# Optimization experiments

Hardware: AMD Instinct MI355X
Metric: run time of the kernel (lower is better)

Reference implementation:

```python
import jax, jax.numpy as jnp
import numpy as np

N_NODES = 100000
N_EDGES = 1600000
HIDDEN = 128
NUM_RBF = 50
NTYPES = 95
CUTOFF = 5.0


def setup_inputs() -> dict:
    key = jax.random.key(0)
    ks = jax.random.split(key, 10)
    z = jax.random.randint(ks[0], (N_NODES,), 0, NTYPES)
    node_feat = jax.random.normal(ks[1], (N_NODES, HIDDEN), dtype=jnp.float32)
    edge_index = jax.random.randint(ks[2], (2, N_EDGES), 0, N_NODES)
    # distances uniform in [0, 6) so some edges fall beyond the 5.0 cutoff
    edge_weight = jax.random.uniform(ks[3], (N_EDGES,), dtype=jnp.float32) * 6.0
    edge_attr = jax.random.normal(ks[4], (N_EDGES, NUM_RBF), dtype=jnp.float32)
    # learned parameters
    emb = jax.random.normal(ks[5], (NTYPES, HIDDEN), dtype=jnp.float32)
    dp_w = jax.random.normal(ks[6], (HIDDEN, NUM_RBF), dtype=jnp.float32) * (1.0 / np.sqrt(NUM_RBF))
    dp_b = jnp.zeros((HIDDEN,), dtype=jnp.float32)
    comb_w = jax.random.normal(ks[7], (HIDDEN, 2 * HIDDEN), dtype=jnp.float32) * (1.0 / np.sqrt(2 * HIDDEN))
    comb_b = jnp.zeros((HIDDEN,), dtype=jnp.float32)
    return {"z": z, "node_feat": node_feat, "edge_index": edge_index,
            "edge_weight": edge_weight, "edge_attr": edge_attr,
            "emb": emb, "dp_w": dp_w, "dp_b": dp_b,
            "comb_w": comb_w, "comb_b": comb_b}


def cosine_cutoff(r, cutoff):
    c = 0.5 * (jnp.cos(r * (jnp.pi / cutoff)) + 1.0)
    return jnp.where(r < cutoff, c, 0.0)


def reference(z, node_feat, edge_index, edge_weight, edge_attr,
              emb, dp_w, dp_b, comb_w, comb_b):
    # distance filter: [E, H]
    C = cosine_cutoff(edge_weight, CUTOFF)
    W = (edge_attr @ dp_w.T + dp_b) * C[:, None]
    # neighbor-type embedding gathered per edge destination
    x_nb = emb[z]                      # [N, H]
    msg = W * x_nb[edge_index[1]]      # [E, H]
    # scatter-add messages to source nodes
    agg = jnp.zeros_like(node_feat).at[edge_index[0]].add(msg)  # [N, H]
    # combine node features with aggregated neighborhood embedding
    out = jnp.concatenate([node_feat, agg], axis=1) @ comb_w.T + comb_b
    return out
```

## Files before the change

### kernel.cpp

```cpp
#include <hip/hip_runtime.h>

#define HIDDEN 128
#define NRBF 50
#define CUTOFF_F 5.0f
#define PI_OVER_CUTOFF 0.6283185307179586f
#define EPB 512
#define B_PITCH 35
#define W_PITCH 66
#define A_PITCH 68

typedef _Float16 half8_t __attribute__((ext_vector_type(8)));
using f32x4_t  = __attribute__((ext_vector_type(4))) float;
using short8_t = __attribute__((ext_vector_type(8))) short;
typedef __attribute__((ext_vector_type(2))) _Float16 hf2;

static __device__ __forceinline__ unsigned int pkh(float a, float b) {
    return __builtin_bit_cast(unsigned int, __builtin_amdgcn_cvt_pkrtz(a, b));
}
static __device__ __forceinline__ float cvlo(unsigned int u) {
    return (float)__builtin_bit_cast(hf2, u)[0];
}
static __device__ __forceinline__ float cvhi(unsigned int u) {
    return (float)__builtin_bit_cast(hf2, u)[1];
}
static __device__ __forceinline__ unsigned int pk_bf16(float a, float b) {
    unsigned int ua = __float_as_uint(a), ub = __float_as_uint(b);
    ua = (ua + 0x7FFFu + ((ua >> 16) & 1u)) >> 16;
    ub = (ub + 0x7FFFu + ((ub >> 16) & 1u)) >> 16;
    return ua | (ub << 16);
}
static __device__ __forceinline__ void loadd16(const int4* p, int t, int* s) {
    int4 q0 = p[t * 4], q1 = p[t * 4 + 1], q2 = p[t * 4 + 2], q3 = p[t * 4 + 3];
    s[0]  = __builtin_amdgcn_readfirstlane(q0.x);
    s[1]  = __builtin_amdgcn_readfirstlane(q0.y);
    s[2]  = __builtin_amdgcn_readfirstlane(q0.z);
    s[3]  = __builtin_amdgcn_readfirstlane(q0.w);
    s[4]  = __builtin_amdgcn_readfirstlane(q1.x);
    s[5]  = __builtin_amdgcn_readfirstlane(q1.y);
    s[6]  = __builtin_amdgcn_readfirstlane(q1.z);
    s[7]  = __builtin_amdgcn_readfirstlane(q1.w);
    s[8]  = __builtin_amdgcn_readfirstlane(q2.x);
    s[9]  = __builtin_amdgcn_readfirstlane(q2.y);
    s[10] = __builtin_amdgcn_readfirstlane(q2.z);
    s[11] = __builtin_amdgcn_readfirstlane(q2.w);
    s[12] = __builtin_amdgcn_readfirstlane(q3.x);
    s[13] = __builtin_amdgcn_readfirstlane(q3.y);
    s[14] = __builtin_amdgcn_readfirstlane(q3.z);
    s[15] = __builtin_amdgcn_readfirstlane(q3.w);
}


__global__ __launch_bounds__(256) void hist_kernel(
    const int* __restrict__ ei, const float* __restrict__ ew,
    int* __restrict__ cnt, int E)
{
    int e = blockIdx.x * 256 + threadIdx.x;
    if (e >= E) return;
    float r = ew[e];
    if (r < CUTOFF_F) atomicAdd(&cnt[ei[e]], 1);
}

__global__ __launch_bounds__(256) void scan1_kernel(
    const int* __restrict__ cnt, int* __restrict__ rowptr,
    int* __restrict__ bsum, int N)
{
    __shared__ int sh[256];
    int t = threadIdx.x, b = blockIdx.x;
    int base = b * 1024 + t * 4;
    int v[4];
#pragma unroll
    for (int j = 0; j < 4; ++j) v[j] = (base + j < N) ? cnt[base + j] : 0;
    int s = v[0] + v[1] + v[2] + v[3];
    sh[t] = s;
    __syncthreads();
    for (int off = 1; off < 256; off <<= 1) {
        int x = (t >= off) ? sh[t - off] : 0;
        __syncthreads();
        sh[t] += x;
        __syncthreads();
    }
    int run = sh[t] - s;
#pragma unroll
    for (int j = 0; j < 4; ++j) {
        if (base + j < N) rowptr[base + j] = run;
        run += v[j];
    }
    if (t == 255) bsum[b] = sh[255];
}

__global__ __launch_bounds__(256) void scan2_kernel(
    int* __restrict__ bsum, int* __restrict__ rowptr, int nb, int N)
{
    __shared__ int sh[256];
    int t = threadIdx.x;
    int v = (t < nb) ? bsum[t] : 0;
    sh[t] = v;
    __syncthreads();
    for (int off = 1; off < 256; off <<= 1) {
        int x = (t >= off) ? sh[t - off] : 0;
        __syncthreads();
        sh[t] += x;
        __syncthreads();
    }
    if (t < nb) bsum[t] = sh[t] - v;
    if (t == 255) rowptr[N] = sh[255];
}

__global__ __launch_bounds__(256) void scan3_kernel(
    int* __restrict__ rowptr, int* __restrict__ woff,
    const int* __restrict__ bsum, int N)
{
    int t = threadIdx.x, b = blockIdx.x;
    int base = b * 1024 + t * 4;
    int off = bsum[b];
#pragma unroll
    for (int j = 0; j < 4; ++j) {
        int i = base + j;
        if (i < N) {
            int r = rowptr[i] + off;
            rowptr[i] = r;
            woff[i] = r;
        }
    }
}

__global__ __launch_bounds__(256) void pad_kernel(
    const int* __restrict__ rowptr, int N,
    int* __restrict__ desc, int* __restrict__ eidA, float* __restrict__ CA)
{
    int M = rowptr[N];
    int t = blockIdx.x * 256 + threadIdx.x;
    if (t < 512) { desc[M + t] = 0; eidA[M + t] = 0; CA[M + t] = 0.f; }
}

__global__ __launch_bounds__(256) void pack_emb(
    const float* __restrict__ emb, unsigned int* __restrict__ embp, int NT)
{
    int i = blockIdx.x * 256 + threadIdx.x;
    if (i >= NT * 64) return;
    int t = i >> 6, j = i & 63;
    embp[i] = pkh(emb[t * HIDDEN + j], emb[t * HIDDEN + j + 64]);
}

__global__ __launch_bounds__(256) void scatter_slim(
    const int* __restrict__ z, const int* __restrict__ ei,
    const float* __restrict__ ew, int* __restrict__ woff,
    int* __restrict__ desc, int* __restrict__ eidA, float* __restrict__ CA,
    int E)
{
    int e = blockIdx.x * 256 + threadIdx.x;
    if (e >= E) return;
    float r = ew[e];
    if (!(r < CUTOFF_F)) return;
    float C = 0.5f * (cosf(r * PI_OVER_CUTOFF) + 1.0f);
    int src = ei[e];
    int dst = ei[E + e];
    int zt  = z[dst];
    int p = atomicAdd(&woff[src], 1);
    desc[p] = src | (zt << 20);
    eidA[p] = e;
    CA[p]   = C;
}

__global__ __launch_bounds__(256) void gather_mfma(
    const int* __restrict__ rowptr, const int* __restrict__ desc,
    const int* __restrict__ eidA, const float* __restrict__ CA,
    const float* __restrict__ ea, const unsigned int* __restrict__ embp,
    const float* __restrict__ dpw, const float* __restrict__ dpb,
    float* __restrict__ agg, int N)
{
    __shared__ unsigned int Blds[128 * B_PITCH];
    __shared__ float        Ast[4][16 * A_PITCH];
    __shared__ unsigned int Wlds[4][16 * W_PITCH];
    int M = rowptr[N];

    int nwg = gridDim.x, orig = blockIdx.x;
    int q = nwg >> 3, r8 = nwg & 7, xcd = orig & 7, sub = orig >> 3;
    int lb = (xcd < r8) ? xcd * (q + 1) + sub
                        : r8 * (q + 1) + (xcd - r8) * q + sub;
    int gbase = lb * EPB;
    if (gbase >= M) return;

    int tid  = threadIdx.x;
    int w    = tid >> 6;
    int lane = tid & 63;
    int c    = lane & 15;
    int g    = lane >> 4;
    int lidx = min(lane, 49);

    for (int idx = tid; idx < 128 * 32; idx += 256) {
        int h = idx >> 5, p = idx & 31;
        unsigned int u = 0u;
        if (p < 25) {
            float2 v = *(const float2*)(dpw + h * NRBF + 2 * p);
            u = pkh(v.x, v.y);
        } else if (p == 25) {
            u = pkh(dpb[h], 0.f);
        }
        Blds[h * B_PITCH + p] = u;
    }
    __syncthreads();

    float*        AstW = Ast[w];
    unsigned int* Ww   = Wlds[w];
    int wbeg = gbase + w * 128;
    if (wbeg >= M) return;

    bool runc;
    if (wbeg == 0) runc = true;
    else runc = ((desc[wbeg - 1] & 0xFFFFF) != (desc[wbeg] & 0xFFFFF));

    const int4* dp = (const int4*)(desc + wbeg);
    const int4* ep = (const int4*)(eidA + wbeg);

    int sd[16], se[16], sdN[16], seN[16];
    float vr[16], vrN[16];

    loadd16(dp, 0, sd);
    loadd16(ep, 0, se);
    float vC = CA[wbeg + c];
#pragma unroll
    for (int j = 0; j < 16; ++j)
        vr[j] = ea[(size_t)(unsigned int)se[j] * NRBF + lidx];
    loadd16(dp, 1, sdN);
    loadd16(ep, 1, seN);
    float vCN = CA[wbeg + 16 + c];

    int   cur = -1;
    float r0 = 0.f, r1 = 0.f;

    for (int t = 0; t < 8; ++t) {
        if (t < 7) {
#pragma unroll
            for (int j = 0; j < 16; ++j)
                vrN[j] = ea[(size_t)(unsigned int)seN[j] * NRBF + lidx];
        }
        unsigned int evp[16];
#pragma unroll
        for (int j = 0; j < 16; ++j)
            evp[j] = embp[(((unsigned int)sd[j]) >> 20) * 64 + lane];

#pragma unroll
        for (int j = 0; j < 16; ++j)
            AstW[j * A_PITCH + lane] = vr[j];

        const float* ab = &AstW[c * A_PITCH];
        float4 f0 = *(const float4*)&ab[g * 8];
        float4 f1 = *(const float4*)&ab[g * 8 + 4];
        uint4 A0u = make_uint4(pkh(vC * f0.x, vC * f0.y), pkh(vC * f0.z, vC * f0.w),
                               pkh(vC * f1.x, vC * f1.y), pkh(vC * f1.z, vC * f1.w));
        uint4 A1u;
        if (g < 2) {
            float4 h0 = *(const float4*)&ab[32 + g * 8];
            float4 h1 = *(const float4*)&ab[36 + g * 8];
            A1u = make_uint4(pkh(vC * h0.x, vC * h0.y), pkh(vC * h0.z, vC * h0.w),
                             pkh(vC * h1.x, vC * h1.y), pkh(vC * h1.z, vC * h1.w));
        } else if (g == 2) {
            float2 hv = *(const float2*)&ab[48];
            A1u = make_uint4(pkh(vC * hv.x, vC * hv.y), pkh(vC, 0.f), 0u, 0u);
        } else {
            A1u = make_uint4(0u, 0u, 0u, 0u);
        }
        half8_t A0 = __builtin_bit_cast(half8_t, A0u);
        half8_t A1 = __builtin_bit_cast(half8_t, A1u);

        f32x4_t acc[8];
#pragma unroll
        for (int nt = 0; nt < 8; ++nt) {
            uint4 b0 = *(const uint4*)&Blds[(nt * 16 + c) * B_PITCH + g * 4];
            uint4 b1 = *(const uint4*)&Blds[(nt * 16 + c) * B_PITCH + 16 + g * 4];
            f32x4_t a = (f32x4_t){0.f, 0.f, 0.f, 0.f};
            a = __builtin_amdgcn_mfma_f32_16x16x32_f16(A0, __builtin_bit_cast(half8_t, b0), a, 0, 0, 0);
            a = __builtin_amdgcn_mfma_f32_16x16x32_f16(A1, __builtin_bit_cast(half8_t, b1), a, 0, 0, 0);
            acc[nt] = a;
        }

#pragma unroll
        for (int m = 0; m < 4; ++m)
#pragma unroll
            for (int r = 0; r < 4; ++r)
                Ww[(g * 4 + r) * W_PITCH + m * 16 + c] = pkh(acc[m][r], acc[m + 4][r]);

        unsigned int wv[16];
#pragma unroll
        for (int e2 = 0; e2 < 16; ++e2)
            wv[e2] = Ww[e2 * W_PITCH + lane];

#pragma unroll
        for (int e2 = 0; e2 < 16; ++e2) {
            int src = sd[e2] & 0xFFFFF;
            if (src != cur) {
                if (cur >= 0) {
                    float* dst = agg + (size_t)cur * HIDDEN + lane;
                    if (runc) {
                        dst[0]  = r0;
                        dst[64] = r1;
                    } else {
                        unsafeAtomicAdd(dst,      r0);
                        unsafeAtomicAdd(dst + 64, r1);
                    }
                    runc = true;
                }
                cur = src; r0 = 0.f; r1 = 0.f;
            }
            r0 = fmaf(cvlo(wv[e2]), cvlo(evp[e2]), r0);
            r1 = fmaf(cvhi(wv[e2]), cvhi(evp[e2]), r1);
        }

        if (t < 7) {
#pragma unroll
            for (int k = 0; k < 16; ++k) { sd[k] = sdN[k]; se[k] = seN[k]; vr[k] = vrN[k]; }
            vC = vCN;
            if (t < 6) {
                loadd16(dp, t + 2, sdN);
                loadd16(ep, t + 2, seN);
                vCN = CA[wbeg + (t + 2) * 16 + c];
            }
        }
    }
    if (cur >= 0) {
        int nxt = desc[wbeg + 128] & 0xFFFFF;
        float* dst = agg + (size_t)cur * HIDDEN + lane;
        if (runc && nxt != cur) {
            dst[0]  = r0;
            dst[64] = r1;
        } else {
            unsafeAtomicAdd(dst,      r0);
            unsafeAtomicAdd(dst + 64, r1);
        }
    }
}

__global__ __launch_bounds__(256) void gather_stream(
    const int* __restrict__ rowptr, const int* __restrict__ desc,
    const float* __restrict__ cC, const int* __restrict__ eidA,
    const float* __restrict__ ea, const float* __restrict__ emb,
    const float* __restrict__ dpw, const float* __restrict__ dpb,
    float* __restrict__ agg, int N, int nwaves)
{
    __shared__ unsigned int sh_ea[4][4][32];
    int lane  = threadIdx.x & 63;
    int wslot = threadIdx.x >> 6;
    int wid = __builtin_amdgcn_readfirstlane((int)((blockIdx.x * blockDim.x + threadIdx.x) >> 6));

    hf2 whA[25], whB[25];
    {
        const float* wr0 = dpw + (size_t)(2 * lane) * NRBF;
        const float* wr1 = wr0 + NRBF;
#pragma unroll
        for (int q = 0; q < 25; ++q) {
            float2 x = *(const float2*)(wr0 + 2 * q);
            float2 y = *(const float2*)(wr1 + 2 * q);
            whA[q] = __builtin_bit_cast(hf2, pkh(x.x, x.y));
            whB[q] = __builtin_bit_cast(hf2, pkh(y.x, y.y));
        }
    }
    float2 db = *(const float2*)(dpb + 2 * lane);

    int M  = rowptr[N];
    int CH = (M + nwaves - 1) / nwaves;
    int c0 = min(wid * CH, M);
    int c1 = min(c0 + CH, M);

    int   cur = -1, run_start = c0;
    float a0 = 0.f, a1 = 0.f;

    for (int i = c0; i < c1; i += 4) {
        int sv[4]; float cf[4]; int ed[4]; float2 ev[4]; float2 eaf[4];
#pragma unroll
        for (int j = 0; j < 4; ++j)
            if (i + j < c1) { sv[j] = desc[i + j]; cf[j] = cC[i + j]; ed[j] = eidA[i + j]; }
#pragma unroll
        for (int j = 0; j < 4; ++j)
            if (i + j < c1) ev[j] = *(const float2*)(emb + (size_t)((unsigned int)sv[j] >> 20) * HIDDEN + 2 * lane);
#pragma unroll
        for (int j = 0; j < 4; ++j)
            if (i + j < c1 && lane < 25) eaf[j] = *(const float2*)(ea + (size_t)ed[j] * NRBF + 2 * lane);
#pragma unroll
        for (int j = 0; j < 4; ++j)
            if (i + j < c1 && lane < 28) {
                unsigned int u = 0u;
                if (lane < 25) u = pkh(eaf[j].x, eaf[j].y);
                sh_ea[wslot][j][lane] = u;
            }
#pragma unroll
        for (int j = 0; j < 4; ++j) {
            if (i + j >= c1) break;
            int src = sv[j] & 0xFFFFF;
            if (src != cur) {
                if (cur >= 0) {
                    int rp0 = rowptr[cur], rp1 = rowptr[cur + 1];
                    float* dst = agg + (size_t)cur * HIDDEN + 2 * lane;
                    if (run_start == rp0 && (i + j) == rp1) {
                        *(float2*)dst = make_float2(a0, a1);
                    } else {
                        unsafeAtomicAdd(dst, a0);
                        unsafeAtomicAdd(dst + 1, a1);
                    }
                }
                cur = src; run_start = i + j; a0 = 0.f; a1 = 0.f;
            }
            float s0 = 0.f, s1 = 0.f;
#pragma unroll
            for (int qq = 0; qq < 6; ++qq) {
                uint4 u = *(const uint4*)&sh_ea[wslot][j][qq * 4];
#pragma unroll
                for (int t = 0; t < 4; ++t) {
                    unsigned int ww = (t == 0) ? u.x : (t == 1) ? u.y : (t == 2) ? u.z : u.w;
                    hf2 e2 = __builtin_bit_cast(hf2, ww);
                    s0 = fmaf((float)e2[0], (float)whA[qq*4+t][0], fmaf((float)e2[1], (float)whA[qq*4+t][1], s0));
                    s1 = fmaf((float)e2[0], (float)whB[qq*4+t][0], fmaf((float)e2[1], (float)whB[qq*4+t][1], s1));
                }
            }
            {
                hf2 e2 = __builtin_bit_cast(hf2, sh_ea[wslot][j][24]);
                s0 = fmaf((float)e2[0], (float)whA[24][0], fmaf((float)e2[1], (float)whA[24][1], s0));
                s1 = fmaf((float)e2[0], (float)whB[24][0], fmaf((float)e2[1], (float)whB[24][1], s1));
            }
            float W0 = (s0 + db.x) * cf[j];
            float W1 = (s1 + db.y) * cf[j];
            a0 = fmaf(W0, ev[j].x, a0);
            a1 = fmaf(W1, ev[j].y, a1);
        }
    }
    if (cur >= 0) {
        int rp0 = rowptr[cur], rp1 = rowptr[cur + 1];
        float* dst = agg + (size_t)cur * HIDDEN + 2 * lane;
        if (run_start == rp0 && c1 == rp1) {
            *(float2*)dst = make_float2(a0, a1);
        } else {
            unsafeAtomicAdd(dst, a0);
            unsafeAtomicAdd(dst + 1, a1);
        }
    }
}

__global__ __launch_bounds__(256) void edge_kernel(
    const int* __restrict__ z, const int* __restrict__ ei,
    const float* __restrict__ ew, const float* __restrict__ ea,
    const float* __restrict__ emb, const float* __restrict__ dpw,
    const float* __restrict__ dpb, float* __restrict__ agg, int E)
{
    int e = blockIdx.x * 256 + threadIdx.x;
    if (e >= E) return;
    float r = ew[e];
    if (!(r < CUTOFF_F)) return;
    float C = 0.5f * (cosf(r * PI_OVER_CUTOFF) + 1.0f);
    int src = ei[e];
    int dst = ei[E + e];
    int zt  = z[dst];
    float av[NRBF];
#pragma unroll
    for (int k = 0; k < NRBF; ++k) av[k] = ea[(size_t)e * NRBF + k];
    const float* er = emb + (size_t)zt * HIDDEN;
    float*       ar = agg + (size_t)src * HIDDEN;
#pragma unroll 2
    for (int h = 0; h < HIDDEN; ++h) {
        const float* wrow = dpw + h * NRBF;
        float s0 = 0.f, s1 = 0.f;
#pragma unroll
        for (int k = 0; k < NRBF; k += 2) {
            s0 = fmaf(av[k],     wrow[k],     s0);
            s1 = fmaf(av[k + 1], wrow[k + 1], s1);
        }
        float w2 = (dpb[h] + s0 + s1) * C;
        unsafeAtomicAdd(&ar[h], w2 * er[h]);
    }
}

__global__ __launch_bounds__(256) void combine_mfma(
    const float* __restrict__ nf, const float* __restrict__ cw,
    const float* __restrict__ cbias, float* out, int N)
{
    __shared__ unsigned int As_u[64 * 20];
    __shared__ unsigned int Bs_u[128 * 20];
    int tid  = threadIdx.x;
    int w    = tid >> 6;
    int lane = tid & 63;
    int c    = lane & 15;
    int g    = lane >> 4;
    int row0 = blockIdx.x * 64;

    f32x4_t acc[8];
#pragma unroll
    for (int q = 0; q < 8; ++q) acc[q] = (f32x4_t){0.f, 0.f, 0.f, 0.f};

    for (int ks = 0; ks < 8; ++ks) {
        const float* src = (ks < 4) ? nf : out;
        int kb = (ks & 3) * 32;
        {
            int r = tid >> 2, kq = tid & 3;
            int row = row0 + r;
            float4 v0 = make_float4(0.f, 0.f, 0.f, 0.f), v1 = v0;
            if (row < N) {
                const float4* p = (const float4*)(src + (size_t)row * HIDDEN + kb + kq * 8);
                v0 = p[0]; v1 = p[1];
            }
            *(uint4*)&As_u[r * 20 + kq * 4] =
                make_uint4(pk_bf16(v0.x, v0.y), pk_bf16(v0.z, v0.w),
                           pk_bf16(v1.x, v1.y), pk_bf16(v1.z, v1.w));
        }
        {
            int j = tid >> 1, hf = tid & 1;
            const float4* p = (const float4*)(cw + (size_t)j * 256 + ks * 32 + hf * 16);
            float4 b0 = p[0], b1 = p[1], b2 = p[2], b3 = p[3];
            *(uint4*)&Bs_u[j * 20 + hf * 8] =
                make_uint4(pk_bf16(b0.x, b0.y), pk_bf16(b0.z, b0.w),
                           pk_bf16(b1.x, b1.y), pk_bf16(b1.z, b1.w));
            *(uint4*)&Bs_u[j * 20 + hf * 8 + 4] =
                make_uint4(pk_bf16(b2.x, b2.y), pk_bf16(b2.z, b2.w),
                           pk_bf16(b3.x, b3.y), pk_bf16(b3.z, b3.w));
        }
        __syncthreads();
        uint4 au = *(const uint4*)&As_u[(w * 16 + c) * 20 + g * 4];
        short8_t af = __builtin_bit_cast(short8_t, au);
#pragma unroll
        for (int cbk = 0; cbk < 8; ++cbk) {
            uint4 bu = *(const uint4*)&Bs_u[(cbk * 16 + c) * 20 + g * 4];
            short8_t bf = __builtin_bit_cast(short8_t, bu);
            acc[cbk] = __builtin_amdgcn_mfma_f32_16x16x32_bf16(af, bf, acc[cbk], 0, 0, 0);
        }
        __syncthreads();
    }
#pragma unroll
    for (int cbk = 0; cbk < 8; ++cbk) {
        float bias = cbias[cbk * 16 + c];
#pragma unroll
        for (int r = 0; r < 4; ++r) {
            int row = row0 + w * 16 + g * 4 + r;
            if (row < N) out[(size_t)row * HIDDEN + cbk * 16 + c] = acc[cbk][r] + bias;
        }
    }
}


extern "C" void kernel_launch(void* const* d_in, const int* in_sizes, int n_in,
                              void* d_out, int out_size, void* d_ws, size_t ws_size,
                              hipStream_t stream)
{
    const int*   z   = (const int*)  d_in[0];
    const float* nf  = (const float*)d_in[1];
    const int*   ei  = (const int*)  d_in[2];
    const float* ew  = (const float*)d_in[3];
    const float* ea  = (const float*)d_in[4];
    const float* emb = (const float*)d_in[5];
    const float* dpw = (const float*)d_in[6];
    const float* dpb = (const float*)d_in[7];
    const float* cw  = (const float*)d_in[8];
    const float* cb  = (const float*)d_in[9];
    float* out = (float*)d_out;

    int N = in_sizes[0];
    int E = in_sizes[3];
    int NT = in_sizes[5] / HIDDEN;

    size_t hdr  = ((size_t)2 * N + 1 + 1024 + 3) & ~(size_t)3;
    size_t Epad = (size_t)E + 512;
    size_t need1 = (hdr + 3 * Epad + (size_t)NT * 64 + 16) * 4;
    size_t need2 = (hdr + (size_t)3 * E) * 4;

    (void)hipMemsetAsync(out, 0, (size_t)N * HIDDEN * sizeof(float), stream);

    int nb1 = (N + 1023) / 1024;

    if (ws_size >= need1) {
        int* rowptr = (int*)d_ws;
        int* woff   = rowptr + (N + 1);
        int* bsum   = woff + N;
        int* desc   = (int*)d_ws + hdr;
        int* eidA   = desc + Epad;
        float* CAa  = (float*)(eidA + Epad);
        unsigned int* embp = (unsigned int*)(CAa + Epad);

        (void)hipMemsetAsync(woff, 0, (size_t)N * 4, stream);
        hist_kernel<<<(E + 255) / 256, 256, 0, stream>>>(ei, ew, woff, E);
        scan1_kernel<<<nb1, 256, 0, stream>>>(woff, rowptr, bsum, N);
        scan2_kernel<<<1, 256, 0, stream>>>(bsum, rowptr, nb1, N);
        scan3_kernel<<<nb1, 256, 0, stream>>>(rowptr, woff, bsum, N);
        pack_emb<<<(NT * 64 + 255) / 256, 256, 0, stream>>>(emb, embp, NT);
        scatter_slim<<<(E + 255) / 256, 256, 0, stream>>>(z, ei, ew, woff,
                                                          desc, eidA, CAa, E);
        pad_kernel<<<2, 256, 0, stream>>>(rowptr, N, desc, eidA, CAa);
        int nblk = (E + EPB - 1) / EPB;
        gather_mfma<<<nblk, 256, 0, stream>>>(rowptr, desc, eidA, CAa, ea,
                                              embp, dpw, dpb, out, N);
    } else if (ws_size >= need2) {
        int* rowptr = (int*)d_ws;
        int* woff   = rowptr + (N + 1);
        int* bsum   = woff + N;
        int* desc   = (int*)d_ws + hdr;
        float* cCA  = (float*)(desc + E);
        int* eidA   = (int*)(cCA + E);

        (void)hipMemsetAsync(woff, 0, (size_t)N * 4, stream);
        hist_kernel<<<(E + 255) / 256, 256, 0, stream>>>(ei, ew, woff, E);
        scan1_kernel<<<nb1, 256, 0, stream>>>(woff, rowptr, bsum, N);
        scan2_kernel<<<1, 256, 0, stream>>>(bsum, rowptr, nb1, N);
        scan3_kernel<<<nb1, 256, 0, stream>>>(rowptr, woff, bsum, N);
        scatter_simple_fallback:
        {
        }
        scatter_slim<<<(E + 255) / 256, 256, 0, stream>>>(z, ei, ew, woff,
                                                          desc, eidA, (float*)cCA, E);
        const int blocks = 2048;
        gather_stream<<<blocks, 256, 0, stream>>>(rowptr, desc, cCA, eidA,
                                                  ea, emb, dpw, dpb, out, N,
                                                  blocks * 4);
    } else {
        edge_kernel<<<(E + 255) / 256, 256, 0, stream>>>(z, ei, ew, ea, emb,
                                                         dpw, dpb, out, E);
    }

    combine_mfma<<<(N + 63) / 64, 256, 0, stream>>>(nf, cw, cb, out, N);
}
```

Measured before the change: 382.9 us.

## Pack edge RBF tile to fp16 in registers and deepen edge_attr prefetch

Restructures the per-wave loop of the gather kernel. Edge-attribute loads are now double-buffered two tiles ahead (vrA/vrB) through a macro body unrolled by two. The A operand is packed to fp16 with a lane shuffle before it goes to LDS, which halves the staging tile and merges it with the W buffer. The cosine-cutoff scale moves from the MFMA input onto the MFMA output, read through LDS. The aim is to hide the scattered edge_attr latency and cut LDS traffic and conversion work. In exchange, the prefetch reads descriptor and edge-id slots past the wave's 128 edges, which relies on padding, and register pressure rises.

```diff
diff --git a/kernel.cpp b/kernel.cpp
--- a/kernel.cpp
+++ b/kernel.cpp
@@ -5,9 +5,9 @@
 #define CUTOFF_F 5.0f
 #define PI_OVER_CUTOFF 0.6283185307179586f
 #define EPB 512
-#define B_PITCH 35
-#define W_PITCH 66
-#define A_PITCH 68
+#define BPITCH 36
+#define APITCH 28
+#define WPITCH 65
 
 typedef _Float16 half8_t __attribute__((ext_vector_type(8)));
 using f32x4_t  = __attribute__((ext_vector_type(4))) float;
@@ -169,9 +169,8 @@
     const float* __restrict__ dpw, const float* __restrict__ dpb,
     float* __restrict__ agg, int N)
 {
-    __shared__ unsigned int Blds[128 * B_PITCH];
-    __shared__ float        Ast[4][16 * A_PITCH];
-    __shared__ unsigned int Wlds[4][16 * W_PITCH];
+    __shared__ unsigned int Blds[128 * BPITCH];
+    __shared__ unsigned int Rsh_all[4][16 * WPITCH];
     int M = rowptr[N];
 
     int nwg = gridDim.x, orig = blockIdx.x;
@@ -184,9 +183,11 @@
     int tid  = threadIdx.x;
     int w    = tid >> 6;
     int lane = tid & 63;
-    int c    = lane & 15;
+    int cc   = lane & 15;
     int g    = lane >> 4;
     int lidx = min(lane, 49);
+    int kk   = lane >> 1;
+    bool wrA = ((lane & 1) == 0) && (lane < 56);
 
     for (int idx = tid; idx < 128 * 32; idx += 256) {
         int h = idx >> 5, p = idx & 31;
@@ -197,12 +198,11 @@
         } else if (p == 25) {
             u = pkh(dpb[h], 0.f);
         }
-        Blds[h * B_PITCH + p] = u;
+        Blds[h * BPITCH + p] = u;
     }
     __syncthreads();
 
-    float*        AstW = Ast[w];
-    unsigned int* Ww   = Wlds[w];
+    unsigned int* Rsh = Rsh_all[w];
     int wbeg = gbase + w * 128;
     if (wbeg >= M) return;
 
@@ -213,111 +213,105 @@
     const int4* dp = (const int4*)(desc + wbeg);
     const int4* ep = (const int4*)(eidA + wbeg);
 
-    int sd[16], se[16], sdN[16], seN[16];
-    float vr[16], vrN[16];
-
-    loadd16(dp, 0, sd);
-    loadd16(ep, 0, se);
-    float vC = CA[wbeg + c];
+    int sd0[16], sd1[16], sp[16];
+    float vrA[16], vrB[16];
+
+    loadd16(dp, 0, sd0);
+    loadd16(dp, 1, sd1);
+    loadd16(ep, 0, sp);
 #pragma unroll
     for (int j = 0; j < 16; ++j)
-        vr[j] = ea[(size_t)(unsigned int)se[j] * NRBF + lidx];
-    loadd16(dp, 1, sdN);
-    loadd16(ep, 1, seN);
-    float vCN = CA[wbeg + 16 + c];
+        vrA[j] = ea[(size_t)(unsigned int)sp[j] * NRBF + lidx];
+    loadd16(ep, 1, sp);
+#pragma unroll
+    for (int j = 0; j < 16; ++j)
+        vrB[j] = ea[(size_t)(unsigned int)sp[j] * NRBF + lidx];
+    loadd16(ep, 2, sp);
 
     int   cur = -1;
     float r0 = 0.f, r1 = 0.f;
 
-    for (int t = 0; t < 8; ++t) {
-        if (t < 7) {
-#pragma unroll
-            for (int j = 0; j < 16; ++j)
-                vrN[j] = ea[(size_t)(unsigned int)seN[j] * NRBF + lidx];
-        }
-        unsigned int evp[16];
-#pragma unroll
-        for (int j = 0; j < 16; ++j)
-            evp[j] = embp[(((unsigned int)sd[j]) >> 20) * 64 + lane];
-
-#pragma unroll
-        for (int j = 0; j < 16; ++j)
-            AstW[j * A_PITCH + lane] = vr[j];
-
-        const float* ab = &AstW[c * A_PITCH];
-        float4 f0 = *(const float4*)&ab[g * 8];
-        float4 f1 = *(const float4*)&ab[g * 8 + 4];
-        uint4 A0u = make_uint4(pkh(vC * f0.x, vC * f0.y), pkh(vC * f0.z, vC * f0.w),
-                               pkh(vC * f1.x, vC * f1.y), pkh(vC * f1.z, vC * f1.w));
-        uint4 A1u;
-        if (g < 2) {
-            float4 h0 = *(const float4*)&ab[32 + g * 8];
-            float4 h1 = *(const float4*)&ab[36 + g * 8];
-            A1u = make_uint4(pkh(vC * h0.x, vC * h0.y), pkh(vC * h0.z, vC * h0.w),
-                             pkh(vC * h1.x, vC * h1.y), pkh(vC * h1.z, vC * h1.w));
-        } else if (g == 2) {
-            float2 hv = *(const float2*)&ab[48];
-            A1u = make_uint4(pkh(vC * hv.x, vC * hv.y), pkh(vC, 0.f), 0u, 0u);
-        } else {
-            A1u = make_uint4(0u, 0u, 0u, 0u);
-        }
-        half8_t A0 = __builtin_bit_cast(half8_t, A0u);
-        half8_t A1 = __builtin_bit_cast(half8_t, A1u);
-
-        f32x4_t acc[8];
-#pragma unroll
-        for (int nt = 0; nt < 8; ++nt) {
-            uint4 b0 = *(const uint4*)&Blds[(nt * 16 + c) * B_PITCH + g * 4];
-            uint4 b1 = *(const uint4*)&Blds[(nt * 16 + c) * B_PITCH + 16 + g * 4];
-            f32x4_t a = (f32x4_t){0.f, 0.f, 0.f, 0.f};
-            a = __builtin_amdgcn_mfma_f32_16x16x32_f16(A0, __builtin_bit_cast(half8_t, b0), a, 0, 0, 0);
-            a = __builtin_amdgcn_mfma_f32_16x16x32_f16(A1, __builtin_bit_cast(half8_t, b1), a, 0, 0, 0);
-            acc[nt] = a;
-        }
-
-#pragma unroll
-        for (int m = 0; m < 4; ++m)
-#pragma unroll
-            for (int r = 0; r < 4; ++r)
-                Ww[(g * 4 + r) * W_PITCH + m * 16 + c] = pkh(acc[m][r], acc[m + 4][r]);
-
-        unsigned int wv[16];
-#pragma unroll
-        for (int e2 = 0; e2 < 16; ++e2)
-            wv[e2] = Ww[e2 * W_PITCH + lane];
-
-#pragma unroll
-        for (int e2 = 0; e2 < 16; ++e2) {
-            int src = sd[e2] & 0xFFFFF;
-            if (src != cur) {
-                if (cur >= 0) {
-                    float* dst = agg + (size_t)cur * HIDDEN + lane;
-                    if (runc) {
-                        dst[0]  = r0;
-                        dst[64] = r1;
-                    } else {
-                        unsafeAtomicAdd(dst,      r0);
-                        unsafeAtomicAdd(dst + 64, r1);
-                    }
-                    runc = true;
-                }
-                cur = src; r0 = 0.f; r1 = 0.f;
-            }
-            r0 = fmaf(cvlo(wv[e2]), cvlo(evp[e2]), r0);
-            r1 = fmaf(cvhi(wv[e2]), cvhi(evp[e2]), r1);
-        }
-
-        if (t < 7) {
-#pragma unroll
-            for (int k = 0; k < 16; ++k) { sd[k] = sdN[k]; se[k] = seN[k]; vr[k] = vrN[k]; }
-            vC = vCN;
-            if (t < 6) {
-                loadd16(dp, t + 2, sdN);
-                loadd16(ep, t + 2, seN);
-                vCN = CA[wbeg + (t + 2) * 16 + c];
-            }
-        }
-    }
+#define GBODY(VRC, T)                                                          \
+{                                                                              \
+    const int t_  = (T);                                                       \
+    const int eb_ = wbeg + t_ * 16;                                            \
+    float Cv_ = CA[eb_ + cc];                                                  \
+    unsigned int evp_[16];                                                     \
+    _Pragma("unroll")                                                          \
+    for (int j = 0; j < 16; ++j)                                               \
+        evp_[j] = embp[(((unsigned int)sd0[j]) >> 20) * 64 + lane];            \
+         \
+    _Pragma("unroll")                                                          \
+    for (int j = 0; j < 16; ++j) {                                             \
+        float pv_ = __shfl_xor(VRC[j], 1);                                     \
+        unsigned int u_ = pkh(VRC[j], pv_);                                    \
+        if (kk == 25) u_ = 0x00003C00u;                                        \
+        else if (kk >= 26) u_ = 0u;                                            \
+        if (wrA) Rsh[j * APITCH + kk] = u_;                                    \
+    }                                                                          \
+                                   \
+    _Pragma("unroll")                                                          \
+    for (int j = 0; j < 16; ++j)                                               \
+        VRC[j] = ea[(size_t)(unsigned int)sp[j] * NRBF + lidx];                \
+                                               \
+    uint4 A0u_ = *(const uint4*)&Rsh[cc * APITCH + 4 * g];                     \
+    uint4 A1u_;                                                                \
+    if (g < 2)       A1u_ = *(const uint4*)&Rsh[cc * APITCH + 16 + 4 * g];     \
+    else if (g == 2) A1u_ = *(const uint4*)&Rsh[cc * APITCH + 24];             \
+    else             A1u_ = make_uint4(0u, 0u, 0u, 0u);                        \
+    half8_t A0_ = __builtin_bit_cast(half8_t, A0u_);                           \
+    half8_t A1_ = __builtin_bit_cast(half8_t, A1u_);                           \
+    f32x4_t acc_[8];                                                           \
+    _Pragma("unroll")                                                          \
+    for (int nt = 0; nt < 8; ++nt) {                                           \
+        uint4 b0_ = *(const uint4*)&Blds[(nt * 16 + cc) * BPITCH + 4 * g];     \
+        uint4 b1_ = *(const uint4*)&Blds[(nt * 16 + cc) * BPITCH + 16 + 4 * g];\
+        f32x4_t a_ = (f32x4_t){0.f, 0.f, 0.f, 0.f};                            \
+        a_ = __builtin_amdgcn_mfma_f32_16x16x32_f16(A0_, __builtin_bit_cast(half8_t, b0_), a_, 0, 0, 0); \
+        a_ = __builtin_amdgcn_mfma_f32_16x16x32_f16(A1_, __builtin_bit_cast(half8_t, b1_), a_, 0, 0, 0); \
+        acc_[nt] = a_;                                                         \
+    }                                                                          \
+                      \
+    _Pragma("unroll")                                                          \
+    for (int m = 0; m < 4; ++m)                                                \
+        _Pragma("unroll")                                                      \
+        for (int r = 0; r < 4; ++r)                                            \
+            Rsh[(g * 4 + r) * WPITCH + m * 16 + cc] = pkh(acc_[m][r], acc_[m + 4][r]); \
+    if (lane < 16) Rsh[lane * WPITCH + 64] = __builtin_bit_cast(unsigned int, Cv_); \
+    unsigned int wv_[16];                                                      \
+    _Pragma("unroll")                                                          \
+    for (int e2 = 0; e2 < 16; ++e2)                                            \
+        wv_[e2] = Rsh[e2 * WPITCH + lane];                                     \
+                                    \
+    _Pragma("unroll")                                                          \
+    for (int e2 = 0; e2 < 16; ++e2) {                                          \
+        int src_ = sd0[e2] & 0xFFFFF;                                          \
+        if (src_ != cur) {                                                     \
+            if (cur >= 0) {                                                    \
+                float* dst_ = agg + (size_t)cur * HIDDEN + lane;               \
+                if (runc) { dst_[0] = r0; dst_[64] = r1; }                     \
+                else { unsafeAtomicAdd(dst_, r0); unsafeAtomicAdd(dst_ + 64, r1); } \
+                runc = true;                                                   \
+            }                                                                  \
+            cur = src_; r0 = 0.f; r1 = 0.f;                                    \
+        }                                                                      \
+        float cf_ = __builtin_bit_cast(float, Rsh[e2 * WPITCH + 64]);          \
+        r0 = fmaf(cf_ * cvlo(wv_[e2]), cvlo(evp_[e2]), r0);                    \
+        r1 = fmaf(cf_ * cvhi(wv_[e2]), cvhi(evp_[e2]), r1);                    \
+    }                                                                          \
+                                                     \
+    _Pragma("unroll")                                                          \
+    for (int j = 0; j < 16; ++j) sd0[j] = sd1[j];                              \
+    loadd16(dp, t_ + 2, sd1);                                                  \
+    loadd16(ep, t_ + 3, sp);                                                   \
+}
+
+    for (int t = 0; t < 8; t += 2) {
+        GBODY(vrA, t);
+        GBODY(vrB, t + 1);
+    }
+#undef GBODY
+
     if (cur >= 0) {
         int nxt = desc[wbeg + 128] & 0xFFFFF;
         float* dst = agg + (size_t)cur * HIDDEN + lane;
@@ -597,11 +591,8 @@
         scan1_kernel<<<nb1, 256, 0, stream>>>(woff, rowptr, bsum, N);
         scan2_kernel<<<1, 256, 0, stream>>>(bsum, rowptr, nb1, N);
         scan3_kernel<<<nb1, 256, 0, stream>>>(rowptr, woff, bsum, N);
-        scatter_simple_fallback:
-        {
-        }
         scatter_slim<<<(E + 255) / 256, 256, 0, stream>>>(z, ei, ew, woff,
-                                                          desc, eidA, (float*)cCA, E);
+                                                          desc, eidA, cCA, E);
         const int blocks = 2048;
         gather_stream<<<blocks, 256, 0, stream>>>(rowptr, desc, cCA, eidA,
                                                   ea, emb, dpw, dpb, out, N,
```

Measured after the change: 401.9 us. 5.0% more time.
